# Performance work log

Measured on AMD Instinct MI355X. Metric: run time of the kernel, lower is better.

Reference implementation:

```python
import jax, jax.numpy as jnp
import numpy as np

BIN = 48
CPG = BIN * 3            # 144 hidden channels
SCALE = 2.0 / (BIN - 1)  # quantization step


def _causal_mask(k, include_center):
    # PixelCNN-style raster causal mask for a k x k kernel
    m = np.zeros((k, k), np.float32)
    c = k // 2
    m[:c, :] = 1.0
    m[c, :c] = 1.0
    if include_center:
        m[c, c] = 1.0
    return jnp.asarray(m)

MASK_NC = _causal_mask(5, False)  # first layer: strictly causal (exclude center)
MASK_C = _causal_mask(5, True)    # hidden/final layers: include center


def mconv(x, w, b, mask):
    # masked 5x5 conv, SAME padding, NCHW / OIHW
    y = jax.lax.conv_general_dilated(x, w * mask, (1, 1), 'SAME',
                                     dimension_numbers=('NCHW', 'OIHW', 'NCHW'))
    return y + b[None, :, None, None]


def setup_inputs() -> dict:
    key = jax.random.key(0)
    ks = jax.random.split(key, 8)
    H, W = 256, 512
    std = 0.02
    # quantized code in [-1, 1] on the bin grid, as produced by the decode loop
    lv = jax.random.randint(ks[0], (1, 1, H, W), 0, BIN)
    x = lv.astype(jnp.float32) * SCALE - 1.0
    return {
        'x': x,
        'w0': jax.random.normal(ks[1], (CPG, 1, 5, 5), jnp.float32) * std,
        'b0': jax.random.normal(ks[2], (CPG,), jnp.float32) * std,
        'wr': jax.random.normal(ks[3], (10, CPG, CPG, 5, 5), jnp.float32) * std,
        'br': jax.random.normal(ks[4], (10, CPG), jnp.float32) * std,
        'wf': jax.random.normal(ks[5], (BIN + 1, CPG, 5, 5), jnp.float32) * std,
        'bf': jax.random.normal(ks[6], (BIN + 1,), jnp.float32) * std,
    }


def reference(x, w0, b0, wr, br, wf, bf):
    # causal conv entropy network (CconvDc stack + 5 residual blocks)
    h = jax.nn.relu(mconv(x, w0, b0, MASK_NC))
    for i in range(5):  # EntropyResidualBlockD x5 (fixed small layer loop)
        y = jax.nn.relu(mconv(h, wr[2 * i], br[2 * i], MASK_C))
        y = jax.nn.relu(mconv(y, wr[2 * i + 1], br[2 * i + 1], MASK_C))
        h = h + y
    logits = mconv(h, wf, bf, MASK_C)            # (1, BIN+1, H, W)
    probs = jax.nn.softmax(logits, axis=1)       # per-pixel symbol distribution (EntropyTable input)

    # tail of forward: importance code -> channel mask -> depth-to-space x2
    tcode = jnp.floor((x + 1.0) / SCALE + 1e-5)  # (1,1,H,W) in [0, BIN-1]
    ch = jnp.arange(BIN * 4, dtype=x.dtype)[None, :, None, None]
    tmask = (ch < tcode * 4.0).astype(x.dtype)   # Imp2mask: (1, 4*BIN, H, W)
    N, C, H, W = tmask.shape
    t = tmask.reshape(N, C // 4, 2, 2, H, W)
    t = t.transpose(0, 1, 4, 2, 5, 3).reshape(N, C // 4, 2 * H, 2 * W)  # Dtow(2)
    return probs, t
```

## Files before the change

### kernel.cpp

```cpp
#include <hip/hip_runtime.h>
#include <hip/hip_bf16.h>
#include <stdint.h>

#define H 256
#define W 512
#define NCG 18
#define AW 520
#define AH 258
#define XB 16
#define ROWB (AW*XB)
#define CGB (AH*ROWB)
#define ACTB ((size_t)NCG*(size_t)CGB)
#define KG 236
#define NCHUNK 59
#define CHUNKB 9216
#define CHUNKFB 4096
#define WPH_B ((size_t)KG*144*16)
#define WPF_B ((size_t)KG*64*16)

typedef float f32x4 __attribute__((ext_vector_type(4)));
typedef short bf16x8 __attribute__((ext_vector_type(8)));

__device__ __forceinline__ float bf2f(unsigned short u) {
  union { unsigned int i; float f; } v; v.i = ((unsigned int)u) << 16; return v.f;
}
__device__ __forceinline__ unsigned short f2bf(float f) {
  __hip_bfloat16 h = __float2bfloat16(f);
  return __builtin_bit_cast(unsigned short, h);
}
__device__ __forceinline__ void gload_lds16(const void* g, void* l) {
  __builtin_amdgcn_global_load_lds(
      (const __attribute__((address_space(1))) unsigned int*)g,
      (__attribute__((address_space(3))) unsigned int*)l, 16, 0, 0);
}

__global__ void k_pack_h(const float* __restrict__ wr, char* __restrict__ wph) {
  int idx = blockIdx.x * 256 + threadIdx.x;
  if (idx >= 10 * 144 * 144) return;
  int ci = idx % 144; int rem = idx / 144; int co = rem % 144; int layer = rem / 144;
  const float* src = wr + (size_t)((layer * 144 + co) * 144 + ci) * 25;
  unsigned short* dstL = (unsigned short*)(wph + (size_t)layer * WPH_B);
  int cig = ci >> 3, cis = ci & 7;
#pragma unroll
  for (int tap = 0; tap < 13; ++tap) {
    int ky = (tap >= 5) + (tap >= 10);
    int kx = tap - ky * 5;
    dstL[((size_t)(cig * 13 + tap) * 144 + co) * 8 + cis] = f2bf(src[ky * 5 + kx]);
  }
}
__global__ void k_pack_f(const float* __restrict__ wf, char* __restrict__ wpf) {
  int idx = blockIdx.x * 256 + threadIdx.x;
  if (idx >= 49 * 144) return;
  int ci = idx % 144; int co = idx / 144;
  const float* src = wf + (size_t)(co * 144 + ci) * 25;
  unsigned short* dst = (unsigned short*)wpf;
  int cig = ci >> 3, cis = ci & 7;
#pragma unroll
  for (int tap = 0; tap < 13; ++tap) {
    int ky = (tap >= 5) + (tap >= 10);
    int kx = tap - ky * 5;
    dst[((size_t)(cig * 13 + tap) * 64 + co) * 8 + cis] = f2bf(src[ky * 5 + kx]);
  }
}
__global__ void k_biaspad(const float* __restrict__ bf, float* __restrict__ bfp) {
  int i = threadIdx.x;
  bfp[i] = (i < 49) ? bf[i] : -1e30f;
}

__global__ void k_zeropad(char* __restrict__ actA, char* __restrict__ actB) {
  int i = blockIdx.x * 256 + threadIdx.x;
  if (i >= 2 * 18 * 2064) return;
  int s = i % 2064; int p = i / 2064; int cig = p % 18; int buf = p / 18;
  char* base = (buf ? actB : actA) + (size_t)cig * CGB;
  int row, colpx;
  if (s < 1040) { row = s / 520; colpx = s - row * 520; }
  else { int s2 = s - 1040; row = 2 + (s2 >> 2); int m = s2 & 3; colpx = (m < 2) ? m : (512 + m); }
  uint4 z; z.x = z.y = z.z = z.w = 0u;
  *(uint4*)(base + (size_t)row * ROWB + (size_t)colpx * 16) = z;
}

__global__ void k_layer0(const float* __restrict__ x, const float* __restrict__ w0,
                         const float* __restrict__ b0, char* __restrict__ act) {
  int i = blockIdx.x * 256 + threadIdx.x;
  int y = i >> 9, xx = i & 511;
  float xv[12];
#pragma unroll
  for (int tp = 0; tp < 12; ++tp) {
    int ky = (tp >= 5) + (tp >= 10);
    int kx = tp - ky * 5;
    int yy = y + ky - 2, xs = xx + kx - 2;
    bool ok = (yy >= 0) && (xs >= 0) && (xs < W);
    xv[tp] = ok ? x[yy * W + xs] : 0.f;
  }
  char* ob = act + (size_t)(y + 2) * ROWB + (size_t)(xx + 2) * XB;
  for (int cg = 0; cg < NCG; ++cg) {
    unsigned int us[4];
#pragma unroll
    for (int h2 = 0; h2 < 4; ++h2) {
      unsigned int lohi = 0;
#pragma unroll
      for (int p = 0; p < 2; ++p) {
        int co = cg * 8 + h2 * 2 + p;
        float a = b0[co];
#pragma unroll
        for (int tp = 0; tp < 12; ++tp) {
          int ky = (tp >= 5) + (tp >= 10);
          int kx = tp - ky * 5;
          a += w0[co * 25 + ky * 5 + kx] * xv[tp];
        }
        a = fmaxf(a, 0.f);
        lohi |= ((unsigned int)f2bf(a)) << (16 * p);
      }
      us[h2] = lohi;
    }
    uint4 v; v.x = us[0]; v.y = us[1]; v.z = us[2]; v.w = us[3];
    *(uint4*)(ob + (size_t)cg * CGB) = v;
  }
}

__global__ __launch_bounds__(256, 4)
void k_conv(const char* __restrict__ in, char* __restrict__ out,
            const char* __restrict__ wp, const float* __restrict__ bias, int res) {
  __shared__ __align__(16) char lA[2][CHUNKB];
  const int tid = threadIdx.x;
  const int wid = tid >> 6, lane = tid & 63;
  const int col = lane & 15, g = lane >> 4;

  int bid = blockIdx.x;
  int xcd = bid & 7, idx = bid >> 3;
  int by = xcd * 8 + (idx >> 4), bx = idx & 15;
  int y = by * 4 + wid, x0 = bx * 32;

  int pxo[2];
#pragma unroll
  for (int t = 0; t < 2; ++t) pxo[t] = (x0 + 16 * t + col) * XB;
  const char* bbase = in + (size_t)y * ROWB;

  f32x4 acc[9][2];
#pragma unroll
  for (int m = 0; m < 9; ++m)
#pragma unroll
    for (int t = 0; t < 2; ++t) acc[m][t] = (f32x4){0.f, 0.f, 0.f, 0.f};

  bf16x8 bA[2], bB[2];

  int tap = g, offc = 0;
  auto bload = [&](bf16x8 (&dst)[2]) __attribute__((always_inline)) {
    int ky = (tap >= 5) + (tap >= 10);
    int kx = tap - ky * 5;
    int off = offc + ky * (int)ROWB + (kx << 4);
#pragma unroll
    for (int t = 0; t < 2; ++t) dst[t] = *(const bf16x8*)(bbase + (size_t)(off + pxo[t]));
    tap += 4; if (tap >= 13) { tap -= 13; offc += (int)CGB; }
  };

  auto stage = [&](char* ldsn, int c) __attribute__((always_inline)) {
    const char* wsrc = wp + (size_t)c * CHUNKB;
#pragma unroll
    for (int j0 = 0; j0 < 3; ++j0) {
      int j = wid + j0 * 4;
      if (j < 9) gload_lds16(wsrc + (size_t)j * 1024 + (lane << 4), ldsn + j * 1024);
    }
  };

  auto domfma = [&](const char* ldsc, bf16x8 (&bcur)[2]) __attribute__((always_inline)) {
    const char* abase = ldsc + ((g * 144 + col) << 4);
    __builtin_amdgcn_s_setprio(1);
#pragma unroll
    for (int m = 0; m < 9; ++m) {
      bf16x8 a = *(const bf16x8*)(abase + m * 256);
#pragma unroll
      for (int t = 0; t < 2; ++t)
        acc[m][t] = __builtin_amdgcn_mfma_f32_16x16x32_bf16(a, bcur[t], acc[m][t], 0, 0, 0);
    }
    __builtin_amdgcn_s_setprio(0);
  };

  auto phase = [&](const char* ldsc, char* ldsn, bf16x8 (&bcur)[2], bf16x8 (&bnext)[2],
                   int c) __attribute__((always_inline)) {
    stage(ldsn, c + 1);
    asm volatile("" ::: "memory");
    bload(bnext);
    asm volatile("" ::: "memory");
    domfma(ldsc, bcur);
    asm volatile("s_waitcnt vmcnt(2)" ::: "memory");
    __builtin_amdgcn_s_barrier();
    asm volatile("" ::: "memory");
  };

  stage(&lA[0][0], 0);
  asm volatile("" ::: "memory");
  bload(bA);
  asm volatile("s_waitcnt vmcnt(0)" ::: "memory");
  __builtin_amdgcn_s_barrier();
  asm volatile("" ::: "memory");

#pragma unroll 1
  for (int c = 0; c < NCHUNK - 1; c += 2) {
    phase(&lA[0][0], &lA[1][0], bA, bB, c);
    phase(&lA[1][0], &lA[0][0], bB, bA, c + 1);
  }
  domfma(&lA[0][0], bA);

  const int sub = (g & 1) * 8;
#pragma unroll
  for (int m = 0; m < 9; ++m) {
    int co0 = m * 16 + (g << 2);
    f32x4 bv = *(const f32x4*)(bias + co0);
    char* ob = out + (size_t)(co0 >> 3) * CGB + (size_t)(y + 2) * ROWB + sub + 32;
#pragma unroll
    for (int t = 0; t < 2; ++t) {
      char* oa = ob + pxo[t];
      float v0 = fmaxf(acc[m][t][0] + bv[0], 0.f);
      float v1 = fmaxf(acc[m][t][1] + bv[1], 0.f);
      float v2 = fmaxf(acc[m][t][2] + bv[2], 0.f);
      float v3 = fmaxf(acc[m][t][3] + bv[3], 0.f);
      if (res) {
        uint2 old = *(const uint2*)oa;
        v0 += bf2f((unsigned short)(old.x & 0xffff));
        v1 += bf2f((unsigned short)(old.x >> 16));
        v2 += bf2f((unsigned short)(old.y & 0xffff));
        v3 += bf2f((unsigned short)(old.y >> 16));
      }
      uint2 st;
      st.x = (unsigned int)f2bf(v0) | ((unsigned int)f2bf(v1) << 16);
      st.y = (unsigned int)f2bf(v2) | ((unsigned int)f2bf(v3) << 16);
      *(uint2*)oa = st;
    }
  }
}

__global__ __launch_bounds__(256, 4)
void k_convf(const char* __restrict__ in, float* __restrict__ probs,
             const char* __restrict__ wp, const float* __restrict__ bfp) {
  __shared__ __align__(16) char lA[2][CHUNKFB];
  const int tid = threadIdx.x;
  const int wid = tid >> 6, lane = tid & 63;
  const int col = lane & 15, g = lane >> 4;

  int bid = blockIdx.x;
  int xcd = bid & 7, idx = bid >> 3;
  int by = xcd * 8 + (idx >> 4), bx = idx & 15;
  int y = by * 4 + wid, x0 = bx * 32;

  int pxo[2];
#pragma unroll
  for (int t = 0; t < 2; ++t) pxo[t] = (x0 + 16 * t + col) * XB;
  const char* bbase = in + (size_t)y * ROWB;

  f32x4 acc[4][2];
#pragma unroll
  for (int m = 0; m < 4; ++m)
#pragma unroll
    for (int t = 0; t < 2; ++t) acc[m][t] = (f32x4){0.f, 0.f, 0.f, 0.f};

  bf16x8 bA[2], bB[2];

  int tap = g, offc = 0;
  auto bload = [&](bf16x8 (&dst)[2]) __attribute__((always_inline)) {
    int ky = (tap >= 5) + (tap >= 10);
    int kx = tap - ky * 5;
    int off = offc + ky * (int)ROWB + (kx << 4);
#pragma unroll
    for (int t = 0; t < 2; ++t) dst[t] = *(const bf16x8*)(bbase + (size_t)(off + pxo[t]));
    tap += 4; if (tap >= 13) { tap -= 13; offc += (int)CGB; }
  };

  auto stage = [&](char* ldsn, int c) __attribute__((always_inline)) {
    if (wid < 4)
      gload_lds16(wp + (size_t)c * CHUNKFB + (size_t)wid * 1024 + (lane << 4),
                  ldsn + wid * 1024);
  };

  auto domfma = [&](const char* ldsc, bf16x8 (&bcur)[2]) __attribute__((always_inline)) {
    const char* abase = ldsc + ((g * 64 + col) << 4);
    __builtin_amdgcn_s_setprio(1);
#pragma unroll
    for (int m = 0; m < 4; ++m) {
      bf16x8 a = *(const bf16x8*)(abase + m * 256);
#pragma unroll
      for (int t = 0; t < 2; ++t)
        acc[m][t] = __builtin_amdgcn_mfma_f32_16x16x32_bf16(a, bcur[t], acc[m][t], 0, 0, 0);
    }
    __builtin_amdgcn_s_setprio(0);
  };

  auto phase = [&](const char* ldsc, char* ldsn, bf16x8 (&bcur)[2], bf16x8 (&bnext)[2],
                   int c) __attribute__((always_inline)) {
    stage(ldsn, c + 1);
    asm volatile("" ::: "memory");
    bload(bnext);
    asm volatile("" ::: "memory");
    domfma(ldsc, bcur);
    asm volatile("s_waitcnt vmcnt(2)" ::: "memory");
    __builtin_amdgcn_s_barrier();
    asm volatile("" ::: "memory");
  };

  stage(&lA[0][0], 0);
  asm volatile("" ::: "memory");
  bload(bA);
  asm volatile("s_waitcnt vmcnt(0)" ::: "memory");
  __builtin_amdgcn_s_barrier();
  asm volatile("" ::: "memory");

#pragma unroll 1
  for (int c = 0; c < NCHUNK - 1; c += 2) {
    phase(&lA[0][0], &lA[1][0], bA, bB, c);
    phase(&lA[1][0], &lA[0][0], bB, bA, c + 1);
  }
  domfma(&lA[0][0], bA);

#pragma unroll
  for (int t = 0; t < 2; ++t) {
    float lg[4][4];
    float mx = -1e30f;
#pragma unroll
    for (int m = 0; m < 4; ++m) {
      f32x4 bv = *(const f32x4*)(bfp + m * 16 + (g << 2));
#pragma unroll
      for (int r = 0; r < 4; ++r) {
        lg[m][r] = acc[m][t][r] + bv[r];
        mx = fmaxf(mx, lg[m][r]);
      }
    }
    mx = fmaxf(mx, __shfl_xor(mx, 16));
    mx = fmaxf(mx, __shfl_xor(mx, 32));
    float s = 0.f;
#pragma unroll
    for (int m = 0; m < 4; ++m)
#pragma unroll
      for (int r = 0; r < 4; ++r) {
        lg[m][r] = __expf(lg[m][r] - mx);
        s += lg[m][r];
      }
    s += __shfl_xor(s, 16);
    s += __shfl_xor(s, 32);
    float inv = 1.f / s;
    int xp = x0 + 16 * t + col;
    float* op = probs + (size_t)y * W + xp;
#pragma unroll
    for (int m = 0; m < 4; ++m)
#pragma unroll
      for (int r = 0; r < 4; ++r) {
        int co = m * 16 + (g << 2) + r;
        if (co < 49) op[(size_t)co * (H * W)] = lg[m][r] * inv;
      }
  }
}

__global__ void k_tmask(const float* __restrict__ x, float* __restrict__ out1) {
  int i = blockIdx.x * 256 + threadIdx.x;
  int yy = i >> 10, xx = i & 1023;
  float xv = x[(yy >> 1) * W + (xx >> 1)];
  float tc = floorf((xv + 1.0f) / (float)(2.0 / 47.0) + 1e-5f);
#pragma unroll 4
  for (int g = 0; g < 48; ++g)
    out1[(size_t)g * (512 * 1024) + i] = ((float)g < tc) ? 1.0f : 0.0f;
}

extern "C" void kernel_launch(void* const* d_in, const int* in_sizes, int n_in,
                              void* d_out, int out_size, void* d_ws, size_t ws_size,
                              hipStream_t stream) {
  const float* x  = (const float*)d_in[0];
  const float* w0 = (const float*)d_in[1];
  const float* b0 = (const float*)d_in[2];
  const float* wr = (const float*)d_in[3];
  const float* br = (const float*)d_in[4];
  const float* wf = (const float*)d_in[5];
  const float* bf = (const float*)d_in[6];

  char* ws   = (char*)d_ws;
  char* actA = ws;
  char* actB = ws + ACTB;
  char* wph  = ws + 2 * ACTB;
  char* wpf  = wph + 10 * WPH_B;
  float* bfp = (float*)(wpf + WPF_B);

  hipMemsetAsync(wph, 0, 10 * WPH_B + WPF_B + 256, stream);
  k_zeropad<<<(2 * 18 * 2064 + 255) / 256, 256, 0, stream>>>(actA, actB);

  k_pack_h<<<(10 * 144 * 144 + 255) / 256, 256, 0, stream>>>(wr, wph);
  k_pack_f<<<(49 * 144 + 255) / 256, 256, 0, stream>>>(wf, wpf);
  k_biaspad<<<1, 64, 0, stream>>>(bf, bfp);

  k_layer0<<<512, 256, 0, stream>>>(x, w0, b0, actA);

  for (int i = 0; i < 5; ++i) {
    k_conv<<<1024, 256, 0, stream>>>(actA, actB, wph + (size_t)(2 * i) * WPH_B,
                                     br + (2 * i) * 144, 0);
    k_conv<<<1024, 256, 0, stream>>>(actB, actA, wph + (size_t)(2 * i + 1) * WPH_B,
                                     br + (2 * i + 1) * 144, 1);
  }

  float* probs = (float*)d_out;
  k_convf<<<1024, 256, 0, stream>>>(actA, probs, wpf, bfp);
  k_tmask<<<2048, 256, 0, stream>>>(x, probs + (size_t)49 * H * W);
}
```

Measured before the change: 750.4 us.

## Retile hidden conv into two-wave blocks splitting output channels over 64-pixel rows

The hidden-layer conv kernel now runs 128-thread blocks, twice as many of them. Each block covers 64 pixels of a single row instead of four rows of 32 pixels. The two waves split the nine 16-channel output tiles between them, five and four, and each wave holds four pixel fragments. The goal is to reuse each LDS weight fragment over more MFMAs and load fewer activation fragments per channel. The cost is uneven work between the two waves and more weight-staging loads per wave, and the wait counts were adjusted to match.

```diff
diff --git a/kernel.cpp b/kernel.cpp
--- a/kernel.cpp
+++ b/kernel.cpp
@@ -118,7 +118,7 @@
   }
 }
 
-__global__ __launch_bounds__(256, 4)
+__global__ __launch_bounds__(128, 4)
 void k_conv(const char* __restrict__ in, char* __restrict__ out,
             const char* __restrict__ wp, const float* __restrict__ bias, int res) {
   __shared__ __align__(16) char lA[2][CHUNKB];
@@ -128,62 +128,65 @@
 
   int bid = blockIdx.x;
   int xcd = bid & 7, idx = bid >> 3;
-  int by = xcd * 8 + (idx >> 4), bx = idx & 15;
-  int y = by * 4 + wid, x0 = bx * 32;
-
-  int pxo[2];
-#pragma unroll
-  for (int t = 0; t < 2; ++t) pxo[t] = (x0 + 16 * t + col) * XB;
+  int y = xcd * 32 + (idx >> 3);
+  int x0 = (idx & 7) * 64;
+
+  int pxo[4];
+#pragma unroll
+  for (int t = 0; t < 4; ++t) pxo[t] = (x0 + 16 * t + col) * XB;
   const char* bbase = in + (size_t)y * ROWB;
 
-  f32x4 acc[9][2];
-#pragma unroll
-  for (int m = 0; m < 9; ++m)
-#pragma unroll
-    for (int t = 0; t < 2; ++t) acc[m][t] = (f32x4){0.f, 0.f, 0.f, 0.f};
-
-  bf16x8 bA[2], bB[2];
+  f32x4 acc[5][4];
+#pragma unroll
+  for (int mt = 0; mt < 5; ++mt)
+#pragma unroll
+    for (int t = 0; t < 4; ++t) acc[mt][t] = (f32x4){0.f, 0.f, 0.f, 0.f};
+
+  bf16x8 bA[4], bB[4];
 
   int tap = g, offc = 0;
-  auto bload = [&](bf16x8 (&dst)[2]) __attribute__((always_inline)) {
+  auto bload = [&](bf16x8 (&dst)[4]) __attribute__((always_inline)) {
     int ky = (tap >= 5) + (tap >= 10);
     int kx = tap - ky * 5;
     int off = offc + ky * (int)ROWB + (kx << 4);
 #pragma unroll
-    for (int t = 0; t < 2; ++t) dst[t] = *(const bf16x8*)(bbase + (size_t)(off + pxo[t]));
+    for (int t = 0; t < 4; ++t) dst[t] = *(const bf16x8*)(bbase + (size_t)(off + pxo[t]));
     tap += 4; if (tap >= 13) { tap -= 13; offc += (int)CGB; }
   };
 
   auto stage = [&](char* ldsn, int c) __attribute__((always_inline)) {
     const char* wsrc = wp + (size_t)c * CHUNKB;
 #pragma unroll
-    for (int j0 = 0; j0 < 3; ++j0) {
-      int j = wid + j0 * 4;
+    for (int j0 = 0; j0 < 5; ++j0) {
+      int j = wid + j0 * 2;
       if (j < 9) gload_lds16(wsrc + (size_t)j * 1024 + (lane << 4), ldsn + j * 1024);
     }
   };
 
-  auto domfma = [&](const char* ldsc, bf16x8 (&bcur)[2]) __attribute__((always_inline)) {
-    const char* abase = ldsc + ((g * 144 + col) << 4);
+  const int mbase = wid * 5;
+  auto domfma = [&](const char* ldsc, bf16x8 (&bcur)[4]) __attribute__((always_inline)) {
+    const char* abase = ldsc + ((g * 144 + mbase * 16 + col) << 4);
     __builtin_amdgcn_s_setprio(1);
 #pragma unroll
-    for (int m = 0; m < 9; ++m) {
-      bf16x8 a = *(const bf16x8*)(abase + m * 256);
-#pragma unroll
-      for (int t = 0; t < 2; ++t)
-        acc[m][t] = __builtin_amdgcn_mfma_f32_16x16x32_bf16(a, bcur[t], acc[m][t], 0, 0, 0);
+    for (int mt = 0; mt < 5; ++mt) {
+      if (mbase + mt < 9) {
+        bf16x8 a = *(const bf16x8*)(abase + mt * 256);
+#pragma unroll
+        for (int t = 0; t < 4; ++t)
+          acc[mt][t] = __builtin_amdgcn_mfma_f32_16x16x32_bf16(a, bcur[t], acc[mt][t], 0, 0, 0);
+      }
     }
     __builtin_amdgcn_s_setprio(0);
   };
 
-  auto phase = [&](const char* ldsc, char* ldsn, bf16x8 (&bcur)[2], bf16x8 (&bnext)[2],
+  auto phase = [&](const char* ldsc, char* ldsn, bf16x8 (&bcur)[4], bf16x8 (&bnext)[4],
                    int c) __attribute__((always_inline)) {
     stage(ldsn, c + 1);
     asm volatile("" ::: "memory");
     bload(bnext);
     asm volatile("" ::: "memory");
     domfma(ldsc, bcur);
-    asm volatile("s_waitcnt vmcnt(2)" ::: "memory");
+    asm volatile("s_waitcnt vmcnt(4)" ::: "memory");
     __builtin_amdgcn_s_barrier();
     asm volatile("" ::: "memory");
   };
@@ -191,7 +194,7 @@
   stage(&lA[0][0], 0);
   asm volatile("" ::: "memory");
   bload(bA);
-  asm volatile("s_waitcnt vmcnt(0)" ::: "memory");
+  asm volatile("s_waitcnt vmcnt(4)" ::: "memory");
   __builtin_amdgcn_s_barrier();
   asm volatile("" ::: "memory");
 
@@ -204,28 +207,30 @@
 
   const int sub = (g & 1) * 8;
 #pragma unroll
-  for (int m = 0; m < 9; ++m) {
-    int co0 = m * 16 + (g << 2);
-    f32x4 bv = *(const f32x4*)(bias + co0);
-    char* ob = out + (size_t)(co0 >> 3) * CGB + (size_t)(y + 2) * ROWB + sub + 32;
-#pragma unroll
-    for (int t = 0; t < 2; ++t) {
-      char* oa = ob + pxo[t];
-      float v0 = fmaxf(acc[m][t][0] + bv[0], 0.f);
-      float v1 = fmaxf(acc[m][t][1] + bv[1], 0.f);
-      float v2 = fmaxf(acc[m][t][2] + bv[2], 0.f);
-      float v3 = fmaxf(acc[m][t][3] + bv[3], 0.f);
-      if (res) {
-        uint2 old = *(const uint2*)oa;
-        v0 += bf2f((unsigned short)(old.x & 0xffff));
-        v1 += bf2f((unsigned short)(old.x >> 16));
-        v2 += bf2f((unsigned short)(old.y & 0xffff));
-        v3 += bf2f((unsigned short)(old.y >> 16));
-      }
-      uint2 st;
-      st.x = (unsigned int)f2bf(v0) | ((unsigned int)f2bf(v1) << 16);
-      st.y = (unsigned int)f2bf(v2) | ((unsigned int)f2bf(v3) << 16);
-      *(uint2*)oa = st;
+  for (int mt = 0; mt < 5; ++mt) {
+    if (mbase + mt < 9) {
+      int co0 = (mbase + mt) * 16 + (g << 2);
+      f32x4 bv = *(const f32x4*)(bias + co0);
+      char* ob = out + (size_t)(co0 >> 3) * CGB + (size_t)(y + 2) * ROWB + sub + 32;
+#pragma unroll
+      for (int t = 0; t < 4; ++t) {
+        char* oa = ob + pxo[t];
+        float v0 = fmaxf(acc[mt][t][0] + bv[0], 0.f);
+        float v1 = fmaxf(acc[mt][t][1] + bv[1], 0.f);
+        float v2 = fmaxf(acc[mt][t][2] + bv[2], 0.f);
+        float v3 = fmaxf(acc[mt][t][3] + bv[3], 0.f);
+        if (res) {
+          uint2 old = *(const uint2*)oa;
+          v0 += bf2f((unsigned short)(old.x & 0xffff));
+          v1 += bf2f((unsigned short)(old.x >> 16));
+          v2 += bf2f((unsigned short)(old.y & 0xffff));
+          v3 += bf2f((unsigned short)(old.y >> 16));
+        }
+        uint2 st;
+        st.x = (unsigned int)f2bf(v0) | ((unsigned int)f2bf(v1) << 16);
+        st.y = (unsigned int)f2bf(v2) | ((unsigned int)f2bf(v3) << 16);
+        *(uint2*)oa = st;
+      }
     }
   }
 }
@@ -387,9 +392,9 @@
   k_layer0<<<512, 256, 0, stream>>>(x, w0, b0, actA);
 
   for (int i = 0; i < 5; ++i) {
-    k_conv<<<1024, 256, 0, stream>>>(actA, actB, wph + (size_t)(2 * i) * WPH_B,
+    k_conv<<<2048, 128, 0, stream>>>(actA, actB, wph + (size_t)(2 * i) * WPH_B,
                                      br + (2 * i) * 144, 0);
-    k_conv<<<1024, 256, 0, stream>>>(actB, actA, wph + (size_t)(2 * i + 1) * WPH_B,
+    k_conv<<<2048, 128, 0, stream>>>(actB, actA, wph + (size_t)(2 * i + 1) * WPH_B,
                                      br + (2 * i + 1) * 144, 1);
   }
 
```

Measured after the change: 1.114 ms. 48.4% more time.

## Switch masked conv stack to FP8 MFMA with bf16 residual side buffer

Applied to the files above, without the earlier changes.

Convolution activations and weights are now stored in FP8 (e4m3), and the main loop uses the 16x16x128 scaled f8f6f4 MFMA in place of bf16 16x16x32. That cuts the K-chunk count from 59 to 15 and halves the activation bytes read per tap. A separate unpadded bf16 copy of the residual stream keeps the skip-connection accumulation at higher precision. The change relayouts weights and activations, enlarges the LDS chunk (lowering launch bounds to 3 blocks per CU) and loosens waitcnt. It risks accuracy loss from FP8 quantization and may not meet output tolerance.

```diff
diff --git a/kernel.cpp b/kernel.cpp
--- a/kernel.cpp
+++ b/kernel.cpp
@@ -7,19 +7,21 @@
 #define NCG 18
 #define AW 520
 #define AH 258
-#define XB 16
-#define ROWB (AW*XB)
-#define CGB (AH*ROWB)
-#define ACTB ((size_t)NCG*(size_t)CGB)
-#define KG 236
-#define NCHUNK 59
-#define CHUNKB 9216
-#define CHUNKFB 4096
-#define WPH_B ((size_t)KG*144*16)
-#define WPF_B ((size_t)KG*64*16)
+#define XB8 8
+#define ROWF8 (AW*XB8)
+#define CGF8 ((size_t)AH*ROWF8)
+#define ACTF8 ((size_t)NCG*CGF8)
+#define CGBR ((size_t)H*W*16)
+#define ACTBF ((size_t)NCG*CGBR)
+#define NCH8 15
+#define CHB8 18432
+#define CHBF8 8192
+#define WPH8 ((size_t)NCH8*CHB8)
+#define WPF8 ((size_t)NCH8*CHBF8)
 
 typedef float f32x4 __attribute__((ext_vector_type(4)));
-typedef short bf16x8 __attribute__((ext_vector_type(8)));
+typedef int   i32x4 __attribute__((ext_vector_type(4)));
+typedef int   i32x8 __attribute__((ext_vector_type(8)));
 
 __device__ __forceinline__ float bf2f(unsigned short u) {
   union { unsigned int i; float f; } v; v.i = ((unsigned int)u) << 16; return v.f;
@@ -27,39 +29,57 @@
 __device__ __forceinline__ unsigned short f2bf(float f) {
   __hip_bfloat16 h = __float2bfloat16(f);
   return __builtin_bit_cast(unsigned short, h);
+}
+__device__ __forceinline__ unsigned char f2e4(float f) {
+  int v = __builtin_amdgcn_cvt_pk_fp8_f32(f, 0.f, 0, false);
+  return (unsigned char)(v & 0xff);
+}
+__device__ __forceinline__ unsigned int pk4e4(float v0, float v1, float v2, float v3) {
+  int p = __builtin_amdgcn_cvt_pk_fp8_f32(v0, v1, 0, false);
+  p = __builtin_amdgcn_cvt_pk_fp8_f32(v2, v3, p, true);
+  return (unsigned int)p;
 }
 __device__ __forceinline__ void gload_lds16(const void* g, void* l) {
   __builtin_amdgcn_global_load_lds(
       (const __attribute__((address_space(1))) unsigned int*)g,
       (__attribute__((address_space(3))) unsigned int*)l, 16, 0, 0);
 }
-
-__global__ void k_pack_h(const float* __restrict__ wr, char* __restrict__ wph) {
+__device__ __forceinline__ f32x4 mfma8(i32x8 a, i32x8 b, f32x4 c) {
+  return __builtin_amdgcn_mfma_scale_f32_16x16x128_f8f6f4(
+      a, b, c, 0, 0, 0, 0x7F7F7F7F, 0, 0x7F7F7F7F);
+}
+
+__global__ void k_pack_h8(const float* __restrict__ wr, char* __restrict__ wph) {
   int idx = blockIdx.x * 256 + threadIdx.x;
   if (idx >= 10 * 144 * 144) return;
   int ci = idx % 144; int rem = idx / 144; int co = rem % 144; int layer = rem / 144;
   const float* src = wr + (size_t)((layer * 144 + co) * 144 + ci) * 25;
-  unsigned short* dstL = (unsigned short*)(wph + (size_t)layer * WPH_B);
-  int cig = ci >> 3, cis = ci & 7;
+  char* dstL = wph + (size_t)layer * WPH8;
+  int m = co >> 4, l_lo = co & 15;
 #pragma unroll
   for (int tap = 0; tap < 13; ++tap) {
     int ky = (tap >= 5) + (tap >= 10);
     int kx = tap - ky * 5;
-    dstL[((size_t)(cig * 13 + tap) * 144 + co) * 8 + cis] = f2bf(src[ky * 5 + kx]);
-  }
-}
-__global__ void k_pack_f(const float* __restrict__ wf, char* __restrict__ wpf) {
+    int k = ((ci >> 3) * 13 + tap) * 8 + (ci & 7);
+    int chunk = k >> 7, kr = k & 127, g = kr >> 5, e = kr & 31;
+    dstL[(size_t)(chunk * 9 + m) * 2048 + (e >> 4) * 1024 + (g * 16 + l_lo) * 16 + (e & 15)]
+        = (char)f2e4(src[ky * 5 + kx]);
+  }
+}
+__global__ void k_pack_f8(const float* __restrict__ wf, char* __restrict__ wpf) {
   int idx = blockIdx.x * 256 + threadIdx.x;
   if (idx >= 49 * 144) return;
   int ci = idx % 144; int co = idx / 144;
   const float* src = wf + (size_t)(co * 144 + ci) * 25;
-  unsigned short* dst = (unsigned short*)wpf;
-  int cig = ci >> 3, cis = ci & 7;
+  int m = co >> 4, l_lo = co & 15;
 #pragma unroll
   for (int tap = 0; tap < 13; ++tap) {
     int ky = (tap >= 5) + (tap >= 10);
     int kx = tap - ky * 5;
-    dst[((size_t)(cig * 13 + tap) * 64 + co) * 8 + cis] = f2bf(src[ky * 5 + kx]);
+    int k = ((ci >> 3) * 13 + tap) * 8 + (ci & 7);
+    int chunk = k >> 7, kr = k & 127, g = kr >> 5, e = kr & 31;
+    wpf[(size_t)(chunk * 4 + m) * 2048 + (e >> 4) * 1024 + (g * 16 + l_lo) * 16 + (e & 15)]
+        = (char)f2e4(src[ky * 5 + kx]);
   }
 }
 __global__ void k_biaspad(const float* __restrict__ bf, float* __restrict__ bfp) {
@@ -67,20 +87,21 @@
   bfp[i] = (i < 49) ? bf[i] : -1e30f;
 }
 
-__global__ void k_zeropad(char* __restrict__ actA, char* __restrict__ actB) {
+__global__ void k_zeropad8(char* __restrict__ a8, char* __restrict__ b8) {
   int i = blockIdx.x * 256 + threadIdx.x;
   if (i >= 2 * 18 * 2064) return;
   int s = i % 2064; int p = i / 2064; int cig = p % 18; int buf = p / 18;
-  char* base = (buf ? actB : actA) + (size_t)cig * CGB;
+  char* base = (buf ? b8 : a8) + (size_t)cig * CGF8;
   int row, colpx;
   if (s < 1040) { row = s / 520; colpx = s - row * 520; }
   else { int s2 = s - 1040; row = 2 + (s2 >> 2); int m = s2 & 3; colpx = (m < 2) ? m : (512 + m); }
-  uint4 z; z.x = z.y = z.z = z.w = 0u;
-  *(uint4*)(base + (size_t)row * ROWB + (size_t)colpx * 16) = z;
+  uint2 z; z.x = 0u; z.y = 0u;
+  *(uint2*)(base + (size_t)row * ROWF8 + (size_t)colpx * 8) = z;
 }
 
 __global__ void k_layer0(const float* __restrict__ x, const float* __restrict__ w0,
-                         const float* __restrict__ b0, char* __restrict__ act) {
+                         const float* __restrict__ b0, char* __restrict__ actbf,
+                         char* __restrict__ act8) {
   int i = blockIdx.x * 256 + threadIdx.x;
   int y = i >> 9, xx = i & 511;
   float xv[12];
@@ -92,36 +113,40 @@
     bool ok = (yy >= 0) && (xs >= 0) && (xs < W);
     xv[tp] = ok ? x[yy * W + xs] : 0.f;
   }
-  char* ob = act + (size_t)(y + 2) * ROWB + (size_t)(xx + 2) * XB;
+  char* obf = actbf + ((size_t)(y * 512 + xx)) * 16;
+  char* ob8 = act8 + (size_t)(y + 2) * ROWF8 + (size_t)(xx + 2) * 8;
   for (int cg = 0; cg < NCG; ++cg) {
-    unsigned int us[4];
-#pragma unroll
-    for (int h2 = 0; h2 < 4; ++h2) {
-      unsigned int lohi = 0;
-#pragma unroll
-      for (int p = 0; p < 2; ++p) {
-        int co = cg * 8 + h2 * 2 + p;
-        float a = b0[co];
-#pragma unroll
-        for (int tp = 0; tp < 12; ++tp) {
-          int ky = (tp >= 5) + (tp >= 10);
-          int kx = tp - ky * 5;
-          a += w0[co * 25 + ky * 5 + kx] * xv[tp];
-        }
-        a = fmaxf(a, 0.f);
-        lohi |= ((unsigned int)f2bf(a)) << (16 * p);
-      }
-      us[h2] = lohi;
-    }
-    uint4 v; v.x = us[0]; v.y = us[1]; v.z = us[2]; v.w = us[3];
-    *(uint4*)(ob + (size_t)cg * CGB) = v;
-  }
-}
-
-__global__ __launch_bounds__(256, 4)
-void k_conv(const char* __restrict__ in, char* __restrict__ out,
-            const char* __restrict__ wp, const float* __restrict__ bias, int res) {
-  __shared__ __align__(16) char lA[2][CHUNKB];
+    float av[8];
+#pragma unroll
+    for (int p = 0; p < 8; ++p) {
+      int co = cg * 8 + p;
+      float a = b0[co];
+#pragma unroll
+      for (int tp = 0; tp < 12; ++tp) {
+        int ky = (tp >= 5) + (tp >= 10);
+        int kx = tp - ky * 5;
+        a += w0[co * 25 + ky * 5 + kx] * xv[tp];
+      }
+      av[p] = fmaxf(a, 0.f);
+    }
+    uint4 vb;
+    vb.x = (unsigned int)f2bf(av[0]) | ((unsigned int)f2bf(av[1]) << 16);
+    vb.y = (unsigned int)f2bf(av[2]) | ((unsigned int)f2bf(av[3]) << 16);
+    vb.z = (unsigned int)f2bf(av[4]) | ((unsigned int)f2bf(av[5]) << 16);
+    vb.w = (unsigned int)f2bf(av[6]) | ((unsigned int)f2bf(av[7]) << 16);
+    *(uint4*)(obf + (size_t)cg * CGBR) = vb;
+    uint2 v8;
+    v8.x = pk4e4(av[0], av[1], av[2], av[3]);
+    v8.y = pk4e4(av[4], av[5], av[6], av[7]);
+    *(uint2*)(ob8 + (size_t)cg * CGF8) = v8;
+  }
+}
+
+__global__ __launch_bounds__(256, 3)
+void k_conv(const char* __restrict__ in, char* __restrict__ out8,
+            char* __restrict__ resbf, const char* __restrict__ wp,
+            const float* __restrict__ bias, int res) {
+  __shared__ __align__(16) char lA[2][CHB8];
   const int tid = threadIdx.x;
   const int wid = tid >> 6, lane = tid & 63;
   const int col = lane & 15, g = lane >> 4;
@@ -133,8 +158,8 @@
 
   int pxo[2];
 #pragma unroll
-  for (int t = 0; t < 2; ++t) pxo[t] = (x0 + 16 * t + col) * XB;
-  const char* bbase = in + (size_t)y * ROWB;
+  for (int t = 0; t < 2; ++t) pxo[t] = (x0 + 16 * t + col) * XB8;
+  const char* bbase = in + (size_t)y * ROWF8;
 
   f32x4 acc[9][2];
 #pragma unroll
@@ -142,48 +167,57 @@
 #pragma unroll
     for (int t = 0; t < 2; ++t) acc[m][t] = (f32x4){0.f, 0.f, 0.f, 0.f};
 
-  bf16x8 bA[2], bB[2];
-
-  int tap = g, offc = 0;
-  auto bload = [&](bf16x8 (&dst)[2]) __attribute__((always_inline)) {
-    int ky = (tap >= 5) + (tap >= 10);
-    int kx = tap - ky * 5;
-    int off = offc + ky * (int)ROWB + (kx << 4);
-#pragma unroll
-    for (int t = 0; t < 2; ++t) dst[t] = *(const bf16x8*)(bbase + (size_t)(off + pxo[t]));
-    tap += 4; if (tap >= 13) { tap -= 13; offc += (int)CGB; }
+  i32x8 bA[2], bB[2];
+
+  int tap = 4 * g, cig = 0;
+  auto bload = [&](i32x8 (&dst)[2]) __attribute__((always_inline)) {
+#pragma unroll
+    for (int s = 0; s < 4; ++s) {
+      int ts = tap + s, cs = cig;
+      if (ts >= 13) { ts -= 13; cs += 1; }
+      if (cs >= 18) { cs = 0; ts = 0; }
+      int ky = (ts >= 5) + (ts >= 10);
+      int kx = ts - ky * 5;
+      int off = cs * (int)CGF8 + ky * (int)ROWF8 + kx * 8;
+#pragma unroll
+      for (int t = 0; t < 2; ++t) {
+        uint2 u = *(const uint2*)(bbase + (size_t)(off + pxo[t]));
+        dst[t][2 * s] = (int)u.x; dst[t][2 * s + 1] = (int)u.y;
+      }
+    }
+    tap += 3; ++cig; if (tap >= 13) { tap -= 13; ++cig; }
   };
 
   auto stage = [&](char* ldsn, int c) __attribute__((always_inline)) {
-    const char* wsrc = wp + (size_t)c * CHUNKB;
-#pragma unroll
-    for (int j0 = 0; j0 < 3; ++j0) {
+    const char* wsrc = wp + (size_t)c * CHB8;
+#pragma unroll
+    for (int j0 = 0; j0 < 5; ++j0) {
       int j = wid + j0 * 4;
-      if (j < 9) gload_lds16(wsrc + (size_t)j * 1024 + (lane << 4), ldsn + j * 1024);
-    }
-  };
-
-  auto domfma = [&](const char* ldsc, bf16x8 (&bcur)[2]) __attribute__((always_inline)) {
-    const char* abase = ldsc + ((g * 144 + col) << 4);
+      if (j < 18) gload_lds16(wsrc + (size_t)j * 1024 + (lane << 4), ldsn + j * 1024);
+    }
+  };
+
+  auto domfma = [&](const char* ldsc, i32x8 (&b)[2]) __attribute__((always_inline)) {
     __builtin_amdgcn_s_setprio(1);
 #pragma unroll
     for (int m = 0; m < 9; ++m) {
-      bf16x8 a = *(const bf16x8*)(abase + m * 256);
-#pragma unroll
-      for (int t = 0; t < 2; ++t)
-        acc[m][t] = __builtin_amdgcn_mfma_f32_16x16x32_bf16(a, bcur[t], acc[m][t], 0, 0, 0);
+      i32x4 lo = *(const i32x4*)(ldsc + m * 2048 + (lane << 4));
+      i32x4 hi = *(const i32x4*)(ldsc + m * 2048 + 1024 + (lane << 4));
+      i32x8 a = __builtin_shufflevector(lo, hi, 0, 1, 2, 3, 4, 5, 6, 7);
+#pragma unroll
+      for (int t = 0; t < 2; ++t) acc[m][t] = mfma8(a, b[t], acc[m][t]);
     }
     __builtin_amdgcn_s_setprio(0);
   };
 
-  auto phase = [&](const char* ldsc, char* ldsn, bf16x8 (&bcur)[2], bf16x8 (&bnext)[2],
+  auto phase = [&](const char* ldsc, char* ldsn, i32x8 (&bcur)[2], i32x8 (&bnext)[2],
                    int c) __attribute__((always_inline)) {
     stage(ldsn, c + 1);
     asm volatile("" ::: "memory");
     bload(bnext);
     asm volatile("" ::: "memory");
     domfma(ldsc, bcur);
-    asm volatile("s_waitcnt vmcnt(2)" ::: "memory");
+    asm volatile("s_waitcnt vmcnt(8)" ::: "memory");
     __builtin_amdgcn_s_barrier();
     asm volatile("" ::: "memory");
   };
@@ -191,41 +225,45 @@
   stage(&lA[0][0], 0);
   asm volatile("" ::: "memory");
   bload(bA);
-  asm volatile("s_waitcnt vmcnt(0)" ::: "memory");
+  asm volatile("s_waitcnt vmcnt(8)" ::: "memory");
   __builtin_amdgcn_s_barrier();
   asm volatile("" ::: "memory");
 
 #pragma unroll 1
-  for (int c = 0; c < NCHUNK - 1; c += 2) {
+  for (int c = 0; c < NCH8 - 1; c += 2) {
     phase(&lA[0][0], &lA[1][0], bA, bB, c);
     phase(&lA[1][0], &lA[0][0], bB, bA, c + 1);
   }
   domfma(&lA[0][0], bA);
 
-  const int sub = (g & 1) * 8;
 #pragma unroll
   for (int m = 0; m < 9; ++m) {
     int co0 = m * 16 + (g << 2);
     f32x4 bv = *(const f32x4*)(bias + co0);
-    char* ob = out + (size_t)(co0 >> 3) * CGB + (size_t)(y + 2) * ROWB + sub + 32;
+    int plane = co0 >> 3;
+    int sub = (g & 1);
 #pragma unroll
     for (int t = 0; t < 2; ++t) {
-      char* oa = ob + pxo[t];
+      int px = x0 + 16 * t + col;
       float v0 = fmaxf(acc[m][t][0] + bv[0], 0.f);
       float v1 = fmaxf(acc[m][t][1] + bv[1], 0.f);
       float v2 = fmaxf(acc[m][t][2] + bv[2], 0.f);
       float v3 = fmaxf(acc[m][t][3] + bv[3], 0.f);
       if (res) {
-        uint2 old = *(const uint2*)oa;
+        char* rb = resbf + (size_t)plane * CGBR + ((size_t)(y * 512 + px)) * 16 + sub * 8;
+        uint2 old = *(const uint2*)rb;
         v0 += bf2f((unsigned short)(old.x & 0xffff));
         v1 += bf2f((unsigned short)(old.x >> 16));
         v2 += bf2f((unsigned short)(old.y & 0xffff));
         v3 += bf2f((unsigned short)(old.y >> 16));
-      }
-      uint2 st;
-      st.x = (unsigned int)f2bf(v0) | ((unsigned int)f2bf(v1) << 16);
-      st.y = (unsigned int)f2bf(v2) | ((unsigned int)f2bf(v3) << 16);
-      *(uint2*)oa = st;
+        uint2 st;
+        st.x = (unsigned int)f2bf(v0) | ((unsigned int)f2bf(v1) << 16);
+        st.y = (unsigned int)f2bf(v2) | ((unsigned int)f2bf(v3) << 16);
+        *(uint2*)rb = st;
+      }
+      char* o8 = out8 + (size_t)plane * CGF8 + (size_t)(y + 2) * ROWF8
+               + (size_t)(px + 2) * 8 + sub * 4;
+      *(unsigned int*)o8 = pk4e4(v0, v1, v2, v3);
     }
   }
 }
@@ -233,7 +271,7 @@
 __global__ __launch_bounds__(256, 4)
 void k_convf(const char* __restrict__ in, float* __restrict__ probs,
              const char* __restrict__ wp, const float* __restrict__ bfp) {
-  __shared__ __align__(16) char lA[2][CHUNKFB];
+  __shared__ __align__(16) char lA[2][CHBF8];
   const int tid = threadIdx.x;
   const int wid = tid >> 6, lane = tid & 63;
   const int col = lane & 15, g = lane >> 4;
@@ -245,8 +283,8 @@
 
   int pxo[2];
 #pragma unroll
-  for (int t = 0; t < 2; ++t) pxo[t] = (x0 + 16 * t + col) * XB;
-  const char* bbase = in + (size_t)y * ROWB;
+  for (int t = 0; t < 2; ++t) pxo[t] = (x0 + 16 * t + col) * XB8;
+  const char* bbase = in + (size_t)y * ROWF8;
 
   f32x4 acc[4][2];
 #pragma unroll
@@ -254,45 +292,57 @@
 #pragma unroll
     for (int t = 0; t < 2; ++t) acc[m][t] = (f32x4){0.f, 0.f, 0.f, 0.f};
 
-  bf16x8 bA[2], bB[2];
-
-  int tap = g, offc = 0;
-  auto bload = [&](bf16x8 (&dst)[2]) __attribute__((always_inline)) {
-    int ky = (tap >= 5) + (tap >= 10);
-    int kx = tap - ky * 5;
-    int off = offc + ky * (int)ROWB + (kx << 4);
-#pragma unroll
-    for (int t = 0; t < 2; ++t) dst[t] = *(const bf16x8*)(bbase + (size_t)(off + pxo[t]));
-    tap += 4; if (tap >= 13) { tap -= 13; offc += (int)CGB; }
+  i32x8 bA[2], bB[2];
+
+  int tap = 4 * g, cig = 0;
+  auto bload = [&](i32x8 (&dst)[2]) __attribute__((always_inline)) {
+#pragma unroll
+    for (int s = 0; s < 4; ++s) {
+      int ts = tap + s, cs = cig;
+      if (ts >= 13) { ts -= 13; cs += 1; }
+      if (cs >= 18) { cs = 0; ts = 0; }
+      int ky = (ts >= 5) + (ts >= 10);
+      int kx = ts - ky * 5;
+      int off = cs * (int)CGF8 + ky * (int)ROWF8 + kx * 8;
+#pragma unroll
+      for (int t = 0; t < 2; ++t) {
+        uint2 u = *(const uint2*)(bbase + (size_t)(off + pxo[t]));
+        dst[t][2 * s] = (int)u.x; dst[t][2 * s + 1] = (int)u.y;
+      }
+    }
+    tap += 3; ++cig; if (tap >= 13) { tap -= 13; ++cig; }
   };
 
   auto stage = [&](char* ldsn, int c) __attribute__((always_inline)) {
-    if (wid < 4)
-      gload_lds16(wp + (size_t)c * CHUNKFB + (size_t)wid * 1024 + (lane << 4),
-                  ldsn + wid * 1024);
-  };
-
-  auto domfma = [&](const char* ldsc, bf16x8 (&bcur)[2]) __attribute__((always_inline)) {
-    const char* abase = ldsc + ((g * 64 + col) << 4);
+    const char* wsrc = wp + (size_t)c * CHBF8;
+#pragma unroll
+    for (int j0 = 0; j0 < 2; ++j0) {
+      int j = wid + j0 * 4;
+      gload_lds16(wsrc + (size_t)j * 1024 + (lane << 4), ldsn + j * 1024);
+    }
+  };
+
+  auto domfma = [&](const char* ldsc, i32x8 (&b)[2]) __attribute__((always_inline)) {
     __builtin_amdgcn_s_setprio(1);
 #pragma unroll
     for (int m = 0; m < 4; ++m) {
-      bf16x8 a = *(const bf16x8*)(abase + m * 256);
-#pragma unroll
-      for (int t = 0; t < 2; ++t)
-        acc[m][t] = __builtin_amdgcn_mfma_f32_16x16x32_bf16(a, bcur[t], acc[m][t], 0, 0, 0);
+      i32x4 lo = *(const i32x4*)(ldsc + m * 2048 + (lane << 4));
+      i32x4 hi = *(const i32x4*)(ldsc + m * 2048 + 1024 + (lane << 4));
+      i32x8 a = __builtin_shufflevector(lo, hi, 0, 1, 2, 3, 4, 5, 6, 7);
+#pragma unroll
+      for (int t = 0; t < 2; ++t) acc[m][t] = mfma8(a, b[t], acc[m][t]);
     }
     __builtin_amdgcn_s_setprio(0);
   };
 
-  auto phase = [&](const char* ldsc, char* ldsn, bf16x8 (&bcur)[2], bf16x8 (&bnext)[2],
+  auto phase = [&](const char* ldsc, char* ldsn, i32x8 (&bcur)[2], i32x8 (&bnext)[2],
                    int c) __attribute__((always_inline)) {
     stage(ldsn, c + 1);
     asm volatile("" ::: "memory");
     bload(bnext);
     asm volatile("" ::: "memory");
     domfma(ldsc, bcur);
-    asm volatile("s_waitcnt vmcnt(2)" ::: "memory");
+    asm volatile("s_waitcnt vmcnt(8)" ::: "memory");
     __builtin_amdgcn_s_barrier();
     asm volatile("" ::: "memory");
   };
@@ -300,12 +350,12 @@
   stage(&lA[0][0], 0);
   asm volatile("" ::: "memory");
   bload(bA);
-  asm volatile("s_waitcnt vmcnt(0)" ::: "memory");
+  asm volatile("s_waitcnt vmcnt(8)" ::: "memory");
   __builtin_amdgcn_s_barrier();
   asm volatile("" ::: "memory");
 
 #pragma unroll 1
-  for (int c = 0; c < NCHUNK - 1; c += 2) {
+  for (int c = 0; c < NCH8 - 1; c += 2) {
     phase(&lA[0][0], &lA[1][0], bA, bB, c);
     phase(&lA[1][0], &lA[0][0], bB, bA, c + 1);
   }
@@ -370,30 +420,31 @@
   const float* wf = (const float*)d_in[5];
   const float* bf = (const float*)d_in[6];
 
-  char* ws   = (char*)d_ws;
-  char* actA = ws;
-  char* actB = ws + ACTB;
-  char* wph  = ws + 2 * ACTB;
-  char* wpf  = wph + 10 * WPH_B;
-  float* bfp = (float*)(wpf + WPF_B);
-
-  hipMemsetAsync(wph, 0, 10 * WPH_B + WPF_B + 256, stream);
-  k_zeropad<<<(2 * 18 * 2064 + 255) / 256, 256, 0, stream>>>(actA, actB);
-
-  k_pack_h<<<(10 * 144 * 144 + 255) / 256, 256, 0, stream>>>(wr, wph);
-  k_pack_f<<<(49 * 144 + 255) / 256, 256, 0, stream>>>(wf, wpf);
+  char* ws    = (char*)d_ws;
+  char* a8    = ws;
+  char* b8    = ws + ACTF8;
+  char* hbf   = ws + 2 * ACTF8;
+  char* wph8  = hbf + ACTBF;
+  char* wpf8  = wph8 + 10 * WPH8;
+  float* bfp  = (float*)(wpf8 + WPF8);
+
+  hipMemsetAsync(wph8, 0, 10 * WPH8 + WPF8 + 256, stream);
+  k_zeropad8<<<(2 * 18 * 2064 + 255) / 256, 256, 0, stream>>>(a8, b8);
+
+  k_pack_h8<<<(10 * 144 * 144 + 255) / 256, 256, 0, stream>>>(wr, wph8);
+  k_pack_f8<<<(49 * 144 + 255) / 256, 256, 0, stream>>>(wf, wpf8);
   k_biaspad<<<1, 64, 0, stream>>>(bf, bfp);
 
-  k_layer0<<<512, 256, 0, stream>>>(x, w0, b0, actA);
+  k_layer0<<<512, 256, 0, stream>>>(x, w0, b0, hbf, a8);
 
   for (int i = 0; i < 5; ++i) {
-    k_conv<<<1024, 256, 0, stream>>>(actA, actB, wph + (size_t)(2 * i) * WPH_B,
+    k_conv<<<1024, 256, 0, stream>>>(a8, b8, hbf, wph8 + (size_t)(2 * i) * WPH8,
                                      br + (2 * i) * 144, 0);
-    k_conv<<<1024, 256, 0, stream>>>(actB, actA, wph + (size_t)(2 * i + 1) * WPH_B,
+    k_conv<<<1024, 256, 0, stream>>>(b8, a8, hbf, wph8 + (size_t)(2 * i + 1) * WPH8,
                                      br + (2 * i + 1) * 144, 1);
   }
 
   float* probs = (float*)d_out;
-  k_convf<<<1024, 256, 0, stream>>>(actA, probs, wpf, bfp);
+  k_convf<<<1024, 256, 0, stream>>>(a8, probs, wpf8, bfp);
   k_tmask<<<2048, 256, 0, stream>>>(x, probs + (size_t)49 * H * W);
 }
```

New measurement: 908.3 us. +21.0%, slower.
